# Performance work log

Measured on AMD Instinct MI355X. Metric: run time of the kernel, lower is better.

## Reference

```python
import jax, jax.numpy as jnp
import numpy as np

# xLSTM '80k' config: 4 blocks (mLSTM at 0,2,3; sLSTM at 1)
B, S, F = 128, 256, 10      # batch, seq (= context_length = forecast_horizon), features
E, NH = 40, 8               # d_model, heads
DH = E // NH                # 5,  sLSTM per-head dim
I = 128                     # mLSTM inner dim = round64(2*E)
QKB = 4; NQK = I // QKB     # q/k/v block-diagonal proj: 32 blocks of 4
MDH = I // NH               # 16, mLSTM per-head dim
FFD = 64                    # gated FFN dim = round64(1.3*E)
K = 4                       # causal conv kernel
NMB = 3                     # number of mLSTM blocks


def layer_norm(x, w, eps=1e-5):
    mu = x.mean(-1, keepdims=True)
    return (x - mu) * jax.lax.rsqrt(x.var(-1, keepdims=True) + eps) * w


def multihead_norm(x, w, nh, eps=1e-5):
    # per-head group norm over D//nh channels, weight only
    b, s, d = x.shape
    xh = x.reshape(b, s, nh, d // nh)
    xh = (xh - xh.mean(-1, keepdims=True)) * jax.lax.rsqrt(xh.var(-1, keepdims=True) + eps)
    return xh.reshape(b, s, d) * w


def causal_conv(x, w, b):
    # depthwise causal conv1d, kernel K; x: (B,S,C), w: (C,K)
    xt = x.transpose(0, 2, 1)
    y = jax.lax.conv_general_dilated(xt, w[:, None, :], (1,), [(K - 1, 0)],
                                     feature_group_count=x.shape[-1],
                                     dimension_numbers=('NCH', 'OIH', 'NCH'))
    return (y + b[None, :, None]).transpose(0, 2, 1)


def headwise(x, w):
    # block-diagonal linear (LinearHeadwiseExpand, no bias): w (nb, bo, bi)
    nb, bo, bi = w.shape
    xh = x.reshape(*x.shape[:-1], nb, bi)
    return jnp.einsum('bsni,noi->bsno', xh, w).reshape(*x.shape[:-1], nb * bo)


def pos_encoding():
    pos = jnp.arange(S, dtype=jnp.float32)[:, None]
    div = jnp.exp(jnp.arange(0, E, 2, dtype=jnp.float32) * (-np.log(10000.0) / E))
    pe = jnp.zeros((S, E), jnp.float32)
    pe = pe.at[:, 0::2].set(jnp.sin(pos * div))
    pe = pe.at[:, 1::2].set(jnp.cos(pos * div))
    return pe


def mlstm_layer(x, up_w, conv_w, conv_b, q_w, k_w, v_w, ig_w, ig_b, fg_w, fg_b, mhn_w, skip, down_w):
    x_m, z = jnp.split(x @ up_w.T, 2, axis=-1)                 # each (B,S,I)
    x_c = jax.nn.silu(causal_conv(x_m, conv_w, conv_b))
    q, k, v = headwise(x_c, q_w), headwise(x_c, k_w), headwise(x_m, v_w)
    gin = jnp.concatenate([q, k, v], axis=-1)                   # (B,S,3I)
    ip = (gin @ ig_w.T + ig_b).transpose(0, 2, 1)               # (B,NH,S)
    fp = (gin @ fg_w.T + fg_b).transpose(0, 2, 1)
    heads = lambda t: t.reshape(B, S, NH, MDH).transpose(0, 2, 1, 3)
    qh, kh, vh = heads(q), heads(k), heads(v)
    # stabilized parallel mLSTM (parallel_stabilized_simple)
    Fc = jnp.cumsum(jax.nn.log_sigmoid(fp), axis=-1)
    log_fg = Fc[..., :, None] - Fc[..., None, :]                # (B,NH,S,S)
    mask = jnp.tril(jnp.ones((S, S), bool))
    log_D = jnp.where(mask, log_fg, -jnp.inf) + ip[..., None, :]
    mD = jnp.max(log_D, axis=-1, keepdims=True)
    D = jnp.exp(log_D - mD)
    qk = jnp.einsum('bhsd,bhtd->bhst', qh, kh) * (MDH ** -0.5)
    C = qk * D
    nrm = jnp.maximum(jnp.abs(C.sum(-1, keepdims=True)), jnp.exp(-mD))
    h = jnp.einsum('bhst,bhtd->bhsd', C / (nrm + 1e-6), vh)
    h = multihead_norm(h.transpose(0, 2, 1, 3).reshape(B, S, I), mhn_w, NH)
    return ((h + skip * x_c) * jax.nn.silu(z)) @ down_w.T


def slstm_layer(x, conv_w, conv_b, wi, wf, wz, wo, R, bias, mhn_w):
    x_c = jax.nn.silu(causal_conv(x, conv_w, conv_b))
    g = lambda inp, w: headwise(inp, w).reshape(B, S, NH, DH)
    # i,f from conv path; z,o from raw input (order i,f,z,o)
    gx = jnp.stack([g(x_c, wi), g(x_c, wf), g(x, wz), g(x, wo)], axis=3)  # (B,S,NH,4,DH)
    gx = gx.transpose(1, 0, 2, 3, 4)                                      # (S,B,NH,4,DH)

    def step(carry, g_t):
        h, c, n, m = carry
        raw = g_t + jnp.einsum('bhd,hgde->bhge', h, R) + bias
        i_r, f_r, z_r, o_r = raw[:, :, 0], raw[:, :, 1], raw[:, :, 2], raw[:, :, 3]
        logfplusm = m + jax.nn.log_sigmoid(f_r)
        m_new = jnp.maximum(i_r, logfplusm)
        ig, fg = jnp.exp(i_r - m_new), jnp.exp(logfplusm - m_new)
        c_new = fg * c + ig * jnp.tanh(z_r)
        n_new = fg * n + ig
        h_new = jax.nn.sigmoid(o_r) * c_new / n_new
        return (h_new, c_new, n_new, m_new), h_new

    z0 = jnp.zeros((B, NH, DH), jnp.float32)
    _, hs = jax.lax.scan(step, (z0, z0, z0, z0), gx)
    return multihead_norm(hs.transpose(1, 0, 2, 3).reshape(B, S, E), mhn_w, NH)


def _forward(x, in_proj_w, in_proj_b, m_ln_w, m_up_w, m_conv_w, m_conv_b, m_q_w, m_k_w, m_v_w,
             m_ig_w, m_ig_b, m_fg_w, m_fg_b, m_mhn_w, m_skip, m_down_w,
             s_ln1_w, s_conv_w, s_conv_b, s_wi, s_wf, s_wz, s_wo, s_R, s_b, s_mhn_w,
             s_ln2_w, s_ff_up_w, s_ff_down_w, post_ln_w, out_w, out_b):
    h = x @ in_proj_w.T + in_proj_b + pos_encoding()
    mb = lambda h, j: h + mlstm_layer(layer_norm(h, m_ln_w[j]), m_up_w[j], m_conv_w[j], m_conv_b[j],
                                      m_q_w[j], m_k_w[j], m_v_w[j], m_ig_w[j], m_ig_b[j],
                                      m_fg_w[j], m_fg_b[j], m_mhn_w[j], m_skip[j], m_down_w[j])
    h = mb(h, 0)                       # block 0: mLSTM
    # block 1: sLSTM + gated FFN (pre-LN residual)
    h = h + slstm_layer(layer_norm(h, s_ln1_w), s_conv_w, s_conv_b, s_wi, s_wf, s_wz, s_wo, s_R, s_b, s_mhn_w)
    gpre, up = jnp.split(layer_norm(h, s_ln2_w) @ s_ff_up_w.T, 2, axis=-1)
    h = h + (jax.nn.gelu(gpre, approximate=False) * up) @ s_ff_down_w.T
    h = mb(h, 1)                       # block 2: mLSTM
    h = mb(h, 2)                       # block 3: mLSTM
    return layer_norm(h, post_ln_w) @ out_w.T + out_b


def setup_inputs():
    ks = iter(jax.random.split(jax.random.key(0), 64))
    rn = lambda shape, fan: jax.random.normal(next(ks), shape, jnp.float32) * (fan ** -0.5)
    d = {}
    d['x'] = jax.random.normal(next(ks), (B, S, F), jnp.float32)
    d['in_proj_w'] = rn((E, F), F); d['in_proj_b'] = jnp.zeros((E,), jnp.float32)
    d['m_ln_w'] = jnp.ones((NMB, E), jnp.float32)
    d['m_up_w'] = rn((NMB, 2 * I, E), E)
    d['m_conv_w'] = rn((NMB, I, K), K); d['m_conv_b'] = jnp.zeros((NMB, I), jnp.float32)
    d['m_q_w'] = rn((NMB, NQK, QKB, QKB), QKB)
    d['m_k_w'] = rn((NMB, NQK, QKB, QKB), QKB)
    d['m_v_w'] = rn((NMB, NQK, QKB, QKB), QKB)
    d['m_ig_w'] = rn((NMB, NH, 3 * I), 3 * I); d['m_ig_b'] = jnp.zeros((NMB, NH), jnp.float32)
    d['m_fg_w'] = rn((NMB, NH, 3 * I), 3 * I); d['m_fg_b'] = 3.0 * jnp.ones((NMB, NH), jnp.float32)
    d['m_mhn_w'] = jnp.ones((NMB, I), jnp.float32); d['m_skip'] = jnp.ones((NMB, I), jnp.float32)
    d['m_down_w'] = rn((NMB, E, I), I)
    d['s_ln1_w'] = jnp.ones((E,), jnp.float32)
    d['s_conv_w'] = rn((E, K), K); d['s_conv_b'] = jnp.zeros((E,), jnp.float32)
    d['s_wi'] = rn((NH, DH, DH), DH); d['s_wf'] = rn((NH, DH, DH), DH)
    d['s_wz'] = rn((NH, DH, DH), DH); d['s_wo'] = rn((NH, DH, DH), DH)
    d['s_R'] = rn((NH, 4, DH, DH), DH); d['s_b'] = jnp.zeros((NH, 4, DH), jnp.float32)
    d['s_mhn_w'] = jnp.ones((E,), jnp.float32); d['s_ln2_w'] = jnp.ones((E,), jnp.float32)
    d['s_ff_up_w'] = rn((2 * FFD, E), E); d['s_ff_down_w'] = rn((E, FFD), FFD)
    d['post_ln_w'] = jnp.ones((E,), jnp.float32)
    d['out_w'] = rn((1, E), E); d['out_b'] = jnp.zeros((1,), jnp.float32)
    return d


def reference(x, in_proj_w, in_proj_b, m_ln_w, m_up_w, m_conv_w, m_conv_b, m_q_w, m_k_w, m_v_w,
              m_ig_w, m_ig_b, m_fg_w, m_fg_b, m_mhn_w, m_skip, m_down_w,
              s_ln1_w, s_conv_w, s_conv_b, s_wi, s_wf, s_wz, s_wo, s_R, s_b, s_mhn_w,
              s_ln2_w, s_ff_up_w, s_ff_down_w, post_ln_w, out_w, out_b):
    return _forward(x, in_proj_w, in_proj_b, m_ln_w, m_up_w, m_conv_w, m_conv_b, m_q_w, m_k_w, m_v_w,
                    m_ig_w, m_ig_b, m_fg_w, m_fg_b, m_mhn_w, m_skip, m_down_w,
                    s_ln1_w, s_conv_w, s_conv_b, s_wi, s_wf, s_wz, s_wo, s_R, s_b, s_mhn_w,
                    s_ln2_w, s_ff_up_w, s_ff_down_w, post_ln_w, out_w, out_b)
```

## Files before the change

### kernel.cpp

```cpp
#include <hip/hip_runtime.h>
#include <math.h>

constexpr int cB = 128, cS = 256, cF = 10, cE = 40, cNH = 8, cDH = 5;
constexpr int cI = 128, cMDH = 16, cK = 4;

typedef __attribute__((ext_vector_type(8))) short short8v;
typedef __attribute__((ext_vector_type(4))) float f32x4;

#define BC8(v, l) __uint_as_float(__builtin_amdgcn_ds_swizzle(__float_as_uint(v), ((l) << 5) | 0x18))

__device__ __forceinline__ short f2bf(float f) {
    unsigned u = __float_as_uint(f);
    u += 0x7FFF + ((u >> 16) & 1);
    return (short)(u >> 16);
}

__global__ __launch_bounds__(256) void init_k(const float* __restrict__ x, const float* __restrict__ w,
                                              const float* __restrict__ b, float* __restrict__ h) {
    int idx = blockIdx.x * 256 + threadIdx.x;
    int e = idx % cE; int bs = idx / cE; int s = bs % cS;
    float acc = b[e];
    const float* xr = x + (size_t)bs * cF;
#pragma unroll
    for (int f = 0; f < cF; ++f) acc += xr[f] * w[e * cF + f];
    int i2 = e >> 1;
    float div = expf(-(float)(2 * i2) * (logf(10000.f) / 40.0f));
    float arg = (float)s * div;
    acc += (e & 1) ? cosf(arg) : sinf(arg);
    h[idx] = acc;
}

__global__ __launch_bounds__(256) void ln_up_k(const float* __restrict__ h, const float* __restrict__ lnw,
                                               const float* __restrict__ upw, float* __restrict__ xmz) {
    __shared__ float lnr[8][cE];
    int row0 = blockIdx.x * 8;
    int tid = threadIdx.x;
    if (tid < 8) {
        const float* r = h + (size_t)(row0 + tid) * cE;
        float mu = 0.f;
        for (int k = 0; k < cE; ++k) mu += r[k];
        mu *= (1.f / cE);
        float va = 0.f;
        for (int k = 0; k < cE; ++k) { float d = r[k] - mu; va += d * d; }
        va *= (1.f / cE);
        float rs = rsqrtf(va + 1e-5f);
        for (int k = 0; k < cE; ++k) lnr[tid][k] = (r[k] - mu) * rs * lnw[k];
    }
    __syncthreads();
    int o = tid;
    float acc[8] = {0, 0, 0, 0, 0, 0, 0, 0};
    for (int k = 0; k < cE; ++k) {
        float wv = upw[o * cE + k];
#pragma unroll
        for (int r = 0; r < 8; ++r) acc[r] += lnr[r][k] * wv;
    }
#pragma unroll
    for (int r = 0; r < 8; ++r) xmz[(size_t)(row0 + r) * 256 + o] = acc[r];
}

template <int C>
__global__ __launch_bounds__(256) void conv_silu_k(const float* __restrict__ in, int instride,
                                                   const float* __restrict__ w, const float* __restrict__ bias,
                                                   float* __restrict__ out) {
    int idx = blockIdx.x * 256 + threadIdx.x;
    int c = idx % C; int bs = idx / C; int s = bs % cS;
    float acc = bias[c];
#pragma unroll
    for (int j = 0; j < cK; ++j) {
        int sj = s - 3 + j;
        if (sj >= 0) acc += in[(size_t)(bs + j - 3) * instride + c] * w[c * cK + j];
    }
    float sg = 1.f / (1.f + __expf(-acc));
    out[idx] = acc * sg;
}

__global__ __launch_bounds__(256) void qkv_k(const float* __restrict__ xc, const float* __restrict__ xmz,
                                             const float* __restrict__ qw, const float* __restrict__ kw,
                                             const float* __restrict__ vw,
                                             float* __restrict__ qb, float* __restrict__ kb, float* __restrict__ vb) {
    int idx = blockIdx.x * 256 + threadIdx.x;
    int c = idx & 127; int bs = idx >> 7;
    int n = c >> 2, o = c & 3;
    const float* xcr = xc + (size_t)bs * cI + n * 4;
    const float* xmr = xmz + (size_t)bs * 256 + n * 4;
    const float* qwp = qw + n * 16 + o * 4;
    const float* kwp = kw + n * 16 + o * 4;
    const float* vwp = vw + n * 16 + o * 4;
    float aq = 0, ak = 0, av = 0;
#pragma unroll
    for (int i = 0; i < 4; ++i) { float a = xcr[i], m = xmr[i]; aq += a * qwp[i]; ak += a * kwp[i]; av += m * vwp[i]; }
    qb[idx] = aq; kb[idx] = ak; vb[idx] = av;
}

__global__ __launch_bounds__(128, 2) void gates_k(const float* __restrict__ qb, const float* __restrict__ kb,
                                                  const float* __restrict__ vb, const float* __restrict__ igw,
                                                  const float* __restrict__ igb, const float* __restrict__ fgw,
                                                  const float* __restrict__ fgb,
                                                  float* __restrict__ ipb, float* __restrict__ fpb) {
    __shared__ float g[32 * 388];
    __shared__ float w[16 * 388];
    int row0 = blockIdx.x * 32;
    int tid = threadIdx.x;

    for (int i = tid; i < 16 * 96; i += 128) {
        int r = i / 96, c4 = i - r * 96;
        const float* src = (r < 8) ? (igw + r * 384) : (fgw + (r - 8) * 384);
        *(float4*)&w[r * 388 + c4 * 4] = ((const float4*)src)[c4];
    }
    for (int i = tid; i < 32 * 96; i += 128) {
        int r = i / 96, c4 = i - r * 96;
        size_t gr = (size_t)(row0 + r) * cI;
        const float4* src = (c4 < 32) ? (const float4*)(qb + gr) + c4
                          : (c4 < 64) ? (const float4*)(kb + gr) + (c4 - 32)
                                      : (const float4*)(vb + gr) + (c4 - 64);
        *(float4*)&g[r * 388 + c4 * 4] = *src;
    }
    __syncthreads();

    int rp = tid >> 3;
    int hp = tid & 7;
    int r0 = 2 * rp, r1 = r0 + 1;
    int o0 = 2 * hp, o1 = o0 + 1;

    const float4* g0p = (const float4*)(g + r0 * 388);
    const float4* g1p = (const float4*)(g + r1 * 388);
    const float4* w0p = (const float4*)(w + o0 * 388);
    const float4* w1p = (const float4*)(w + o1 * 388);

    float a00 = 0.f, a01 = 0.f, a10 = 0.f, a11 = 0.f;
#pragma unroll 4
    for (int c4 = 0; c4 < 96; ++c4) {
        float4 gv0 = g0p[c4], gv1 = g1p[c4];
        float4 wv0 = w0p[c4], wv1 = w1p[c4];
        a00 = fmaf(gv0.x, wv0.x, a00); a00 = fmaf(gv0.y, wv0.y, a00);
        a00 = fmaf(gv0.z, wv0.z, a00); a00 = fmaf(gv0.w, wv0.w, a00);
        a01 = fmaf(gv0.x, wv1.x, a01); a01 = fmaf(gv0.y, wv1.y, a01);
        a01 = fmaf(gv0.z, wv1.z, a01); a01 = fmaf(gv0.w, wv1.w, a01);
        a10 = fmaf(gv1.x, wv0.x, a10); a10 = fmaf(gv1.y, wv0.y, a10);
        a10 = fmaf(gv1.z, wv0.z, a10); a10 = fmaf(gv1.w, wv0.w, a10);
        a11 = fmaf(gv1.x, wv1.x, a11); a11 = fmaf(gv1.y, wv1.y, a11);
        a11 = fmaf(gv1.z, wv1.z, a11); a11 = fmaf(gv1.w, wv1.w, a11);
    }

    int h0 = o0 & 7, wch0 = o0 >> 3;
    int h1 = o1 & 7, wch1 = o1 >> 3;
    float b0 = wch0 ? fgb[h0] : igb[h0];
    float b1 = wch1 ? fgb[h1] : igb[h1];
    int grow0 = row0 + r0, grow1 = row0 + r1;
    int bb0 = grow0 >> 8, ss0 = grow0 & 255;
    int bb1 = grow1 >> 8, ss1 = grow1 & 255;
    float* d00 = (wch0 ? fpb : ipb) + (size_t)(bb0 * cNH + h0) * cS + ss0;
    float* d01 = (wch1 ? fpb : ipb) + (size_t)(bb0 * cNH + h1) * cS + ss0;
    float* d10 = (wch0 ? fpb : ipb) + (size_t)(bb1 * cNH + h0) * cS + ss1;
    float* d11 = (wch1 ? fpb : ipb) + (size_t)(bb1 * cNH + h1) * cS + ss1;
    *d00 = a00 + b0; *d01 = a01 + b1; *d10 = a10 + b0; *d11 = a11 + b1;
}

constexpr int QKW = 24;
constexpr int VTW = 264;
constexpr int CBW = 280;

__global__ __launch_bounds__(256, 2) void attn_k(const float* __restrict__ qg, const float* __restrict__ kg,
                                                 const float* __restrict__ vg, const float* __restrict__ ipg,
                                                 const float* __restrict__ fpg, float* __restrict__ hatt) {
    int bh = blockIdx.x; int b = bh >> 3, h = bh & 7;
    int tid = threadIdx.x;
    int wid = tid >> 6, lane = tid & 63;
    int colL = lane & 15, grp = lane >> 4;

    __shared__ float sEA[cS], sMx[cS], sFc[cS];
    __shared__ short sQ[cS * QKW], sK[cS * QKW];
    __shared__ short sVt[cMDH * VTW];
    __shared__ short sC[4][16 * CBW];

    {
        const float4 fp4 = ((const float4*)(fpg + (size_t)bh * cS))[lane];
        const float4 ip4 = ((const float4*)(ipg + (size_t)bh * cS))[lane];
        float fpa[4] = {fp4.x, fp4.y, fp4.z, fp4.w};
        float ipa[4] = {ip4.x, ip4.y, ip4.z, ip4.w};
        float p[4];
        float run = 0.f;
#pragma unroll
        for (int i = 0; i < 4; ++i) {
            float xx = fpa[i];
            float lsg = fminf(xx, 0.f) - log1pf(expf(-fabsf(xx)));
            run += lsg; p[i] = run;
        }
        float cum = p[3];
#pragma unroll
        for (int off = 1; off < 64; off <<= 1) { float t = __shfl_up(cum, off); if (lane >= off) cum += t; }
        float excl = cum - p[3];
        float aa[4];
#pragma unroll
        for (int i = 0; i < 4; ++i) {
            float fcv = excl + p[i];
            aa[i] = ipa[i] - fcv;
            sFc[lane * 4 + i] = fcv;
            sEA[lane * 4 + i] = __expf(aa[i]);
        }
        float mq[4]; mq[0] = aa[0];
#pragma unroll
        for (int i = 1; i < 4; ++i) mq[i] = fmaxf(mq[i - 1], aa[i]);
        float cm = mq[3];
#pragma unroll
        for (int off = 1; off < 64; off <<= 1) { float t = __shfl_up(cm, off); if (lane >= off) cm = fmaxf(cm, t); }
        float exm = __shfl_up(cm, 1);
        if (lane == 0) exm = -3.0e38f;
#pragma unroll
        for (int i = 0; i < 4; ++i) sMx[lane * 4 + i] = fmaxf(exm, mq[i]);
    }

    {
        int t = tid;
        const float4* qp = (const float4*)(qg + ((size_t)(b * cS) + t) * cI + h * cMDH);
        const float4* kp = (const float4*)(kg + ((size_t)(b * cS) + t) * cI + h * cMDH);
        const float4* vp = (const float4*)(vg + ((size_t)(b * cS) + t) * cI + h * cMDH);
        float4 q0 = qp[0], q1 = qp[1], q2 = qp[2], q3 = qp[3];
        float4 k0 = kp[0], k1 = kp[1], k2 = kp[2], k3 = kp[3];
        float4 v0 = vp[0], v1 = vp[1], v2 = vp[2], v3 = vp[3];
        short8v qa, qbv, ka, kbv;
        qa[0] = f2bf(q0.x); qa[1] = f2bf(q0.y); qa[2] = f2bf(q0.z); qa[3] = f2bf(q0.w);
        qa[4] = f2bf(q1.x); qa[5] = f2bf(q1.y); qa[6] = f2bf(q1.z); qa[7] = f2bf(q1.w);
        qbv[0] = f2bf(q2.x); qbv[1] = f2bf(q2.y); qbv[2] = f2bf(q2.z); qbv[3] = f2bf(q2.w);
        qbv[4] = f2bf(q3.x); qbv[5] = f2bf(q3.y); qbv[6] = f2bf(q3.z); qbv[7] = f2bf(q3.w);
        ka[0] = f2bf(k0.x); ka[1] = f2bf(k0.y); ka[2] = f2bf(k0.z); ka[3] = f2bf(k0.w);
        ka[4] = f2bf(k1.x); ka[5] = f2bf(k1.y); ka[6] = f2bf(k1.z); ka[7] = f2bf(k1.w);
        kbv[0] = f2bf(k2.x); kbv[1] = f2bf(k2.y); kbv[2] = f2bf(k2.z); kbv[3] = f2bf(k2.w);
        kbv[4] = f2bf(k3.x); kbv[5] = f2bf(k3.y); kbv[6] = f2bf(k3.z); kbv[7] = f2bf(k3.w);
        *(short8v*)(sQ + t * QKW) = qa;
        *(short8v*)(sQ + t * QKW + 8) = qbv;
        *(short8v*)(sK + t * QKW) = ka;
        *(short8v*)(sK + t * QKW + 8) = kbv;
        sVt[0 * VTW + t] = f2bf(v0.x);  sVt[1 * VTW + t] = f2bf(v0.y);
        sVt[2 * VTW + t] = f2bf(v0.z);  sVt[3 * VTW + t] = f2bf(v0.w);
        sVt[4 * VTW + t] = f2bf(v1.x);  sVt[5 * VTW + t] = f2bf(v1.y);
        sVt[6 * VTW + t] = f2bf(v1.z);  sVt[7 * VTW + t] = f2bf(v1.w);
        sVt[8 * VTW + t] = f2bf(v2.x);  sVt[9 * VTW + t] = f2bf(v2.y);
        sVt[10 * VTW + t] = f2bf(v2.z); sVt[11 * VTW + t] = f2bf(v2.w);
        sVt[12 * VTW + t] = f2bf(v3.x); sVt[13 * VTW + t] = f2bf(v3.y);
        sVt[14 * VTW + t] = f2bf(v3.z); sVt[15 * VTW + t] = f2bf(v3.w);
    }
    __syncthreads();

    const short one_bf = (short)0x3F80;
    short8v ones = {one_bf, one_bf, one_bf, one_bf, one_bf, one_bf, one_bf, one_bf};
    short8v kz = {0, 0, 0, 0, 0, 0, 0, 0};
    short* Cb = sC[wid];

    for (int sti = 0; sti < 4; ++sti) {
        int st = wid + sti * 4;
        int s0 = st * 16;

        float eMx4[4], flr4[4];
#pragma unroll
        for (int j = 0; j < 4; ++j) {
            int sg = s0 + grp * 4 + j;
            eMx4[j] = 0.25f * __expf(-sMx[sg]);
            flr4[j] = __expf(-(sFc[sg] + sMx[sg]));
        }

        if ((st & 1) == 0) {
#pragma unroll
            for (int z = 0; z < 4; ++z) {
                int idx = lane * 4 + z;
                Cb[(idx >> 4) * CBW + (st + 1) * 16 + (idx & 15)] = 0;
            }
        }

        short8v aQ = (grp < 2) ? *(const short8v*)(sQ + (s0 + colL) * QKW + grp * 8) : kz;

        for (int tt = 0; tt <= st; ++tt) {
            int t0 = tt * 16;
            short8v bK = (grp < 2) ? *(const short8v*)(sK + (t0 + colL) * QKW + grp * 8) : kz;
            f32x4 zacc = {0.f, 0.f, 0.f, 0.f};
            f32x4 d = __builtin_amdgcn_mfma_f32_16x16x32_bf16(aQ, bK, zacc, 0, 0, 0);
            float ea = sEA[t0 + colL];
#pragma unroll
            for (int j = 0; j < 4; ++j) {
                float v = d[j] * (ea * eMx4[j]);
                if (tt == st) v = (colL <= grp * 4 + j) ? v : 0.f;
                Cb[(grp * 4 + j) * CBW + t0 + colL] = f2bf(v);
            }
        }

        __builtin_amdgcn_s_barrier();
        f32x4 hacc = {0.f, 0.f, 0.f, 0.f};
        f32x4 sacc = {0.f, 0.f, 0.f, 0.f};
        int nch = (st + 2) >> 1;
        for (int c = 0; c < nch; ++c) {
            int tc = c * 32;
            short8v aC = *(const short8v*)(Cb + colL * CBW + tc + grp * 8);
            short8v bV = *(const short8v*)(sVt + colL * VTW + tc + grp * 8);
            hacc = __builtin_amdgcn_mfma_f32_16x16x32_bf16(aC, bV, hacc, 0, 0, 0);
            sacc = __builtin_amdgcn_mfma_f32_16x16x32_bf16(aC, ones, sacc, 0, 0, 0);
        }

#pragma unroll
        for (int j = 0; j < 4; ++j) {
            int sg = s0 + grp * 4 + j;
            float nrm = fmaxf(fabsf(sacc[j]), flr4[j]) + 1e-6f;
            hatt[((size_t)(b * cS) + sg) * cI + h * cMDH + colL] = hacc[j] / nrm;
        }
    }
}

__global__ __launch_bounds__(320) void down_mhn_k(const float* __restrict__ hatt, const float* __restrict__ xc,
                                                  const float* __restrict__ xmz, const float* __restrict__ mhnw,
                                                  const float* __restrict__ skip, const float* __restrict__ dw,
                                                  float* __restrict__ h) {
    __shared__ float yl[8 * 128];
    int row0 = blockIdx.x * 8;
    int tid = threadIdx.x;
    for (int i = tid; i < 1024; i += 320) yl[i] = hatt[(size_t)row0 * cI + i];
    __syncthreads();
    if (tid < 64) {
        int r = tid >> 3, hh = tid & 7;
        int row = row0 + r;
        float* g = yl + r * 128 + hh * 16;
        float xv[16];
        float mu = 0.f;
#pragma unroll
        for (int d = 0; d < 16; ++d) { xv[d] = g[d]; mu += xv[d]; }
        mu *= (1.f / 16);
        float va = 0.f;
#pragma unroll
        for (int d = 0; d < 16; ++d) { float dd = xv[d] - mu; va += dd * dd; }
        va *= (1.f / 16);
        float rs = rsqrtf(va + 1e-5f);
        const float* xcr = xc + (size_t)row * cI + hh * 16;
        const float* zr  = xmz + (size_t)row * 256 + 128 + hh * 16;
#pragma unroll
        for (int d = 0; d < 16; ++d) {
            int i = hh * 16 + d;
            float z = zr[d];
            float sg = 1.f / (1.f + __expf(-z));
            g[d] = ((xv[d] - mu) * rs * mhnw[i] + skip[i] * xcr[d]) * (z * sg);
        }
    }
    __syncthreads();
    int r = tid / 40, e = tid % 40;
    const float* dr = dw + e * cI;
    const float* yr = yl + r * cI;
    float acc = 0.f;
    for (int i = 0; i < cI; ++i) acc += yr[i] * dr[i];
    h[(size_t)(row0 + r) * cE + e] += acc;
}

__global__ __launch_bounds__(256) void ln_rows_k(const float* __restrict__ h, const float* __restrict__ w,
                                                 float* __restrict__ out) {
    int rid = blockIdx.x * 256 + threadIdx.x;
    const float* r = h + (size_t)rid * cE;
    float mu = 0;
    for (int k = 0; k < cE; ++k) mu += r[k];
    mu *= (1.f / cE);
    float va = 0;
    for (int k = 0; k < cE; ++k) { float d = r[k] - mu; va += d * d; }
    va *= (1.f / cE);
    float rs = rsqrtf(va + 1e-5f);
    float* o = out + (size_t)rid * cE;
    for (int k = 0; k < cE; ++k) o[k] = (r[k] - mu) * rs * w[k];
}

__global__ __launch_bounds__(256) void sgates_k(const float* __restrict__ xcs, const float* __restrict__ ln1,
                                                const float* __restrict__ wi, const float* __restrict__ wf,
                                                const float* __restrict__ wz, const float* __restrict__ wo,
                                                float* __restrict__ gall) {
    int idx = blockIdx.x * 256 + threadIdx.x;
    int g = idx & 3; int r1 = idx >> 2;
    int e = r1 % 5; int r2 = r1 / 5;
    int bh = r2 & 1023; int s = r2 >> 10;
    int b = bh >> 3, h = bh & 7;
    const float* in = (g < 2) ? xcs : ln1;
    const float* w = (g == 0) ? wi : (g == 1) ? wf : (g == 2) ? wz : wo;
    const float* ir = in + ((size_t)(b * cS) + s) * cE + h * cDH;
    const float* wp = w + h * 25 + e * 5;
    float acc = 0.f;
#pragma unroll
    for (int i = 0; i < 5; ++i) acc += ir[i] * wp[i];
    gall[idx] = acc;
}

__global__ __launch_bounds__(64) void scan_k(const float* __restrict__ gall, const float* __restrict__ R,
                                             const float* __restrict__ bias, const float* __restrict__ mhnw,
                                             float* __restrict__ hbuf) {
    int lane = threadIdx.x;
    int grp = lane >> 3;
    int e = lane & 7;
    int ee = e < 5 ? e : 4;
    int bh = blockIdx.x * 8 + grp;
    int h = bh & 7;

    __shared__ float sOut[8][1285];

    float Rr[4][5];
#pragma unroll
    for (int g = 0; g < 4; ++g)
#pragma unroll
        for (int d = 0; d < 5; ++d) Rr[g][d] = R[h * 100 + g * 25 + d * 5 + ee];
    float bg[4];
#pragma unroll
    for (int g = 0; g < 4; ++g) bg[g] = bias[h * 20 + g * 5 + ee];
    float wmh = mhnw[h * 5 + ee];

    const float4* gp = (const float4*)gall + ((size_t)bh * 5 + ee);

    float4 rg[16];
#pragma unroll
    for (int j = 0; j < 16; ++j) rg[j] = gp[(size_t)j * 5120];

    float cstate = 0.f, nstate = 0.f, mstate = 0.f;
    float hs0 = 0.f, hs1 = 0.f, hs2 = 0.f, hs3 = 0.f, hs4 = 0.f;

    for (int t = 0; t < cS; t += 16) {
#pragma unroll
        for (int j = 0; j < 16; ++j) {
            float4 g4 = rg[j];
            rg[j] = gp[(size_t)(t + j + 16) * 5120];

            float ir = g4.x + bg[0], fr = g4.y + bg[1], zr = g4.z + bg[2], orr = g4.w + bg[3];
            ir = fmaf(hs0, Rr[0][0], ir); fr = fmaf(hs0, Rr[1][0], fr);
            zr = fmaf(hs0, Rr[2][0], zr); orr = fmaf(hs0, Rr[3][0], orr);
            ir = fmaf(hs1, Rr[0][1], ir); fr = fmaf(hs1, Rr[1][1], fr);
            zr = fmaf(hs1, Rr[2][1], zr); orr = fmaf(hs1, Rr[3][1], orr);
            ir = fmaf(hs2, Rr[0][2], ir); fr = fmaf(hs2, Rr[1][2], fr);
            zr = fmaf(hs2, Rr[2][2], zr); orr = fmaf(hs2, Rr[3][2], orr);
            ir = fmaf(hs3, Rr[0][3], ir); fr = fmaf(hs3, Rr[1][3], fr);
            zr = fmaf(hs3, Rr[2][3], zr); orr = fmaf(hs3, Rr[3][3], orr);
            ir = fmaf(hs4, Rr[0][4], ir); fr = fmaf(hs4, Rr[1][4], fr);
            zr = fmaf(hs4, Rr[2][4], zr); orr = fmaf(hs4, Rr[3][4], orr);

            float lsg = fminf(fr, 0.f) - __logf(1.f + __expf(-fabsf(fr)));
            float lfm = mstate + lsg;
            float mn = fmaxf(ir, lfm);
            float ig = __expf(ir - mn), fg = __expf(lfm - mn);
            float th = 1.f - 2.f * __builtin_amdgcn_rcpf(__expf(2.f * zr) + 1.f);
            float cn = fg * cstate + ig * th;
            float nn = fg * nstate + ig;
            float sg = __builtin_amdgcn_rcpf(1.f + __expf(-orr));
            float hn = sg * cn * __builtin_amdgcn_rcpf(nn);
            cstate = cn; nstate = nn; mstate = mn;

            hs0 = BC8(hn, 0); hs1 = BC8(hn, 1); hs2 = BC8(hn, 2);
            hs3 = BC8(hn, 3); hs4 = BC8(hn, 4);
            float mu = ((hs0 + hs1) + (hs2 + hs3) + hs4) * 0.2f;
            float d0 = hs0 - mu, d1 = hs1 - mu, d2 = hs2 - mu, d3 = hs3 - mu, d4 = hs4 - mu;
            float va = (d0 * d0 + d1 * d1 + d2 * d2 + d3 * d3 + d4 * d4) * 0.2f;
            float rs = __builtin_amdgcn_rsqf(va + 1e-5f);
            if (e < 5) sOut[grp][(t + j) * 5 + e] = (hn - mu) * rs * wmh;
        }
    }
    __syncthreads();

    for (int i = lane; i < 8 * 1280; i += 64) {
        int c = i / 1280;
        int r = i - c * 1280;
        int tt = r / 5, e2 = r - tt * 5;
        int bh2 = blockIdx.x * 8 + c;
        int b2 = bh2 >> 3, h2 = bh2 & 7;
        float* hp = hbuf + ((size_t)b2 * cS + tt) * cE + h2 * cDH + e2;
        *hp += sOut[c][r];
    }
}

__global__ __launch_bounds__(256) void ff1_k(const float* __restrict__ h, const float* __restrict__ lnw,
                                             const float* __restrict__ upw, float* __restrict__ ff) {
    __shared__ float lnr[4][cE];
    int row0 = blockIdx.x * 4;
    int tid = threadIdx.x;
    if (tid < 4) {
        const float* r = h + (size_t)(row0 + tid) * cE;
        float mu = 0;
        for (int k = 0; k < cE; ++k) mu += r[k];
        mu *= (1.f / cE);
        float va = 0;
        for (int k = 0; k < cE; ++k) { float d = r[k] - mu; va += d * d; }
        va *= (1.f / cE);
        float rs = rsqrtf(va + 1e-5f);
        for (int k = 0; k < cE; ++k) lnr[tid][k] = (r[k] - mu) * rs * lnw[k];
    }
    __syncthreads();
    int r = tid >> 6, f = tid & 63;
    float a = 0, u = 0;
    for (int k = 0; k < cE; ++k) {
        float xv = lnr[r][k];
        a += xv * upw[f * cE + k];
        u += xv * upw[(64 + f) * cE + k];
    }
    float g = 0.5f * a * (1.f + erff(a * 0.70710678118f));
    ff[(size_t)(row0 + r) * 64 + f] = g * u;
}

__global__ __launch_bounds__(320) void ff2_k(const float* __restrict__ ff, const float* __restrict__ dw,
                                             float* __restrict__ h) {
    __shared__ float fl[8 * 64];
    int row0 = blockIdx.x * 8;
    for (int i = threadIdx.x; i < 512; i += 320) fl[i] = ff[(size_t)row0 * 64 + i];
    __syncthreads();
    int r = threadIdx.x / 40, e = threadIdx.x % 40;
    const float* dr = dw + e * 64;
    const float* fr = fl + r * 64;
    float acc = 0.f;
    for (int i = 0; i < 64; ++i) acc += fr[i] * dr[i];
    h[(size_t)(row0 + r) * cE + e] += acc;
}

__global__ __launch_bounds__(256) void final_k(const float* __restrict__ h, const float* __restrict__ lnw,
                                               const float* __restrict__ ow, const float* __restrict__ ob,
                                               float* __restrict__ out) {
    int rid = blockIdx.x * 256 + threadIdx.x;
    const float* r = h + (size_t)rid * cE;
    float mu = 0;
    for (int k = 0; k < cE; ++k) mu += r[k];
    mu *= (1.f / cE);
    float va = 0;
    for (int k = 0; k < cE; ++k) { float d = r[k] - mu; va += d * d; }
    va *= (1.f / cE);
    float rs = rsqrtf(va + 1e-5f);
    float acc = ob[0];
    for (int k = 0; k < cE; ++k) acc += (r[k] - mu) * rs * lnw[k] * ow[k];
    out[rid] = acc;
}

extern "C" void kernel_launch(void* const* d_in, const int* in_sizes, int n_in,
                              void* d_out, int out_size, void* d_ws, size_t ws_size,
                              hipStream_t stream) {
    const float* x        = (const float*)d_in[0];
    const float* in_w     = (const float*)d_in[1];
    const float* in_b     = (const float*)d_in[2];
    const float* m_ln_w   = (const float*)d_in[3];
    const float* m_up_w   = (const float*)d_in[4];
    const float* m_conv_w = (const float*)d_in[5];
    const float* m_conv_b = (const float*)d_in[6];
    const float* m_q_w    = (const float*)d_in[7];
    const float* m_k_w    = (const float*)d_in[8];
    const float* m_v_w    = (const float*)d_in[9];
    const float* m_ig_w   = (const float*)d_in[10];
    const float* m_ig_b   = (const float*)d_in[11];
    const float* m_fg_w   = (const float*)d_in[12];
    const float* m_fg_b   = (const float*)d_in[13];
    const float* m_mhn_w  = (const float*)d_in[14];
    const float* m_skip   = (const float*)d_in[15];
    const float* m_down_w = (const float*)d_in[16];
    const float* s_ln1_w  = (const float*)d_in[17];
    const float* s_conv_w = (const float*)d_in[18];
    const float* s_conv_b = (const float*)d_in[19];
    const float* s_wi     = (const float*)d_in[20];
    const float* s_wf     = (const float*)d_in[21];
    const float* s_wz     = (const float*)d_in[22];
    const float* s_wo     = (const float*)d_in[23];
    const float* s_R      = (const float*)d_in[24];
    const float* s_bias   = (const float*)d_in[25];
    const float* s_mhn_w  = (const float*)d_in[26];
    const float* s_ln2_w  = (const float*)d_in[27];
    const float* s_ff_up  = (const float*)d_in[28];
    const float* s_ff_dn  = (const float*)d_in[29];
    const float* post_ln_w= (const float*)d_in[30];
    const float* out_w    = (const float*)d_in[31];
    const float* out_b    = (const float*)d_in[32];

    float* ws   = (float*)d_ws;
    float* h    = ws;
    float* xmz  = h + 1310720;
    float* xc   = xmz + 8388608;
    float* qb   = xc + 4194304;
    float* kb   = qb + 4194304;
    float* vb   = kb + 4194304;
    float* ipb  = vb + 4194304;
    float* fpb  = ipb + 262144;
    float* hatt = fpb + 262144;
    float* lnbuf = xmz;
    float* xcs   = xmz + 1310720;
    float* gall  = xmz + 2621440;
    float* ffbuf = xmz;

    init_k<<<5120, 256, 0, stream>>>(x, in_w, in_b, h);

    auto mlstm = [&](int j) {
        ln_up_k<<<4096, 256, 0, stream>>>(h, m_ln_w + j * cE, m_up_w + (size_t)j * 256 * cE, xmz);
        conv_silu_k<128><<<16384, 256, 0, stream>>>(xmz, 256, m_conv_w + j * cI * cK, m_conv_b + j * cI, xc);
        qkv_k<<<16384, 256, 0, stream>>>(xc, xmz, m_q_w + j * 512, m_k_w + j * 512, m_v_w + j * 512, qb, kb, vb);
        gates_k<<<1024, 128, 0, stream>>>(qb, kb, vb, m_ig_w + j * cNH * 384, m_ig_b + j * cNH,
                                          m_fg_w + j * cNH * 384, m_fg_b + j * cNH, ipb, fpb);
        attn_k<<<1024, 256, 0, stream>>>(qb, kb, vb, ipb, fpb, hatt);
        down_mhn_k<<<4096, 320, 0, stream>>>(hatt, xc, xmz, m_mhn_w + j * cI, m_skip + j * cI,
                                             m_down_w + j * cE * cI, h);
    };

    mlstm(0);

    ln_rows_k<<<128, 256, 0, stream>>>(h, s_ln1_w, lnbuf);
    conv_silu_k<40><<<5120, 256, 0, stream>>>(lnbuf, 40, s_conv_w, s_conv_b, xcs);
    sgates_k<<<20480, 256, 0, stream>>>(xcs, lnbuf, s_wi, s_wf, s_wz, s_wo, gall);
    scan_k<<<128, 64, 0, stream>>>(gall, s_R, s_bias, s_mhn_w, h);

    ff1_k<<<8192, 256, 0, stream>>>(h, s_ln2_w, s_ff_up, ffbuf);
    ff2_k<<<4096, 320, 0, stream>>>(ffbuf, s_ff_dn, h);

    mlstm(1);
    mlstm(2);

    final_k<<<128, 256, 0, stream>>>(h, post_ln_w, out_w, out_b, (float*)d_out);
}
```

Baseline: 892.7 us.

## Retile ln_up, widen gates block, balance attn tiles, drop per-tile barrier

ln_up_k now handles 16 rows per block and stages the up-projection weight transposed in shared memory, so the inner loop reads weights from LDS instead of strided global loads. gates_k runs 256 threads, one output row per thread pair, with two interleaved accumulators. attn_k gives each wave a balanced set of causal tiles (wid, 7-wid, 8+wid, 15-wid) instead of a strided set, and removes a workgroup barrier in the tile loop. The larger LDS footprint in ln_up_k may lower occupancy, and dropping the barrier relies on each wave using only its own Cb buffer.

```diff
diff --git a/kernel.cpp b/kernel.cpp
--- a/kernel.cpp
+++ b/kernel.cpp
@@ -32,10 +32,19 @@
 
 __global__ __launch_bounds__(256) void ln_up_k(const float* __restrict__ h, const float* __restrict__ lnw,
                                                const float* __restrict__ upw, float* __restrict__ xmz) {
-    __shared__ float lnr[8][cE];
-    int row0 = blockIdx.x * 8;
+    __shared__ float lnr[16][cE];
+    __shared__ float wT[cE * 257];
+    int row0 = blockIdx.x * 16;
     int tid = threadIdx.x;
-    if (tid < 8) {
+    for (int j = tid; j < 2560; j += 256) {
+        float4 v = ((const float4*)upw)[j];
+        int o = j / 10, kq = (j - o * 10) * 4;
+        wT[(kq + 0) * 257 + o] = v.x;
+        wT[(kq + 1) * 257 + o] = v.y;
+        wT[(kq + 2) * 257 + o] = v.z;
+        wT[(kq + 3) * 257 + o] = v.w;
+    }
+    if (tid < 16) {
         const float* r = h + (size_t)(row0 + tid) * cE;
         float mu = 0.f;
         for (int k = 0; k < cE; ++k) mu += r[k];
@@ -48,14 +57,16 @@
     }
     __syncthreads();
     int o = tid;
-    float acc[8] = {0, 0, 0, 0, 0, 0, 0, 0};
+    float acc[16];
+#pragma unroll
+    for (int r = 0; r < 16; ++r) acc[r] = 0.f;
     for (int k = 0; k < cE; ++k) {
-        float wv = upw[o * cE + k];
-#pragma unroll
-        for (int r = 0; r < 8; ++r) acc[r] += lnr[r][k] * wv;
-    }
-#pragma unroll
-    for (int r = 0; r < 8; ++r) xmz[(size_t)(row0 + r) * 256 + o] = acc[r];
+        float wv = wT[k * 257 + o];
+#pragma unroll
+        for (int r = 0; r < 16; ++r) acc[r] = fmaf(lnr[r][k], wv, acc[r]);
+    }
+#pragma unroll
+    for (int r = 0; r < 16; ++r) xmz[(size_t)(row0 + r) * 256 + o] = acc[r];
 }
 
 template <int C>
@@ -92,7 +103,7 @@
     qb[idx] = aq; kb[idx] = ak; vb[idx] = av;
 }
 
-__global__ __launch_bounds__(128, 2) void gates_k(const float* __restrict__ qb, const float* __restrict__ kb,
+__global__ __launch_bounds__(256, 2) void gates_k(const float* __restrict__ qb, const float* __restrict__ kb,
                                                   const float* __restrict__ vb, const float* __restrict__ igw,
                                                   const float* __restrict__ igb, const float* __restrict__ fgw,
                                                   const float* __restrict__ fgb,
@@ -102,12 +113,12 @@
     int row0 = blockIdx.x * 32;
     int tid = threadIdx.x;
 
-    for (int i = tid; i < 16 * 96; i += 128) {
+    for (int i = tid; i < 16 * 96; i += 256) {
         int r = i / 96, c4 = i - r * 96;
         const float* src = (r < 8) ? (igw + r * 384) : (fgw + (r - 8) * 384);
         *(float4*)&w[r * 388 + c4 * 4] = ((const float4*)src)[c4];
     }
-    for (int i = tid; i < 32 * 96; i += 128) {
+    for (int i = tid; i < 32 * 96; i += 256) {
         int r = i / 96, c4 = i - r * 96;
         size_t gr = (size_t)(row0 + r) * cI;
         const float4* src = (c4 < 32) ? (const float4*)(qb + gr) + c4
@@ -119,41 +130,38 @@
 
     int rp = tid >> 3;
     int hp = tid & 7;
-    int r0 = 2 * rp, r1 = r0 + 1;
     int o0 = 2 * hp, o1 = o0 + 1;
 
-    const float4* g0p = (const float4*)(g + r0 * 388);
-    const float4* g1p = (const float4*)(g + r1 * 388);
+    const float4* gp = (const float4*)(g + rp * 388);
     const float4* w0p = (const float4*)(w + o0 * 388);
     const float4* w1p = (const float4*)(w + o1 * 388);
 
-    float a00 = 0.f, a01 = 0.f, a10 = 0.f, a11 = 0.f;
-#pragma unroll 4
-    for (int c4 = 0; c4 < 96; ++c4) {
-        float4 gv0 = g0p[c4], gv1 = g1p[c4];
-        float4 wv0 = w0p[c4], wv1 = w1p[c4];
-        a00 = fmaf(gv0.x, wv0.x, a00); a00 = fmaf(gv0.y, wv0.y, a00);
-        a00 = fmaf(gv0.z, wv0.z, a00); a00 = fmaf(gv0.w, wv0.w, a00);
-        a01 = fmaf(gv0.x, wv1.x, a01); a01 = fmaf(gv0.y, wv1.y, a01);
-        a01 = fmaf(gv0.z, wv1.z, a01); a01 = fmaf(gv0.w, wv1.w, a01);
-        a10 = fmaf(gv1.x, wv0.x, a10); a10 = fmaf(gv1.y, wv0.y, a10);
-        a10 = fmaf(gv1.z, wv0.z, a10); a10 = fmaf(gv1.w, wv0.w, a10);
-        a11 = fmaf(gv1.x, wv1.x, a11); a11 = fmaf(gv1.y, wv1.y, a11);
-        a11 = fmaf(gv1.z, wv1.z, a11); a11 = fmaf(gv1.w, wv1.w, a11);
-    }
+    float a0e = 0.f, a0o = 0.f, a1e = 0.f, a1o = 0.f;
+#pragma unroll 2
+    for (int c4 = 0; c4 < 96; c4 += 2) {
+        float4 gv0 = gp[c4], gv1 = gp[c4 + 1];
+        float4 wa0 = w0p[c4], wa1 = w0p[c4 + 1];
+        float4 wb0 = w1p[c4], wb1 = w1p[c4 + 1];
+        a0e = fmaf(gv0.x, wa0.x, a0e); a0e = fmaf(gv0.y, wa0.y, a0e);
+        a0e = fmaf(gv0.z, wa0.z, a0e); a0e = fmaf(gv0.w, wa0.w, a0e);
+        a1e = fmaf(gv0.x, wb0.x, a1e); a1e = fmaf(gv0.y, wb0.y, a1e);
+        a1e = fmaf(gv0.z, wb0.z, a1e); a1e = fmaf(gv0.w, wb0.w, a1e);
+        a0o = fmaf(gv1.x, wa1.x, a0o); a0o = fmaf(gv1.y, wa1.y, a0o);
+        a0o = fmaf(gv1.z, wa1.z, a0o); a0o = fmaf(gv1.w, wa1.w, a0o);
+        a1o = fmaf(gv1.x, wb1.x, a1o); a1o = fmaf(gv1.y, wb1.y, a1o);
+        a1o = fmaf(gv1.z, wb1.z, a1o); a1o = fmaf(gv1.w, wb1.w, a1o);
+    }
+    float a0 = a0e + a0o, a1 = a1e + a1o;
 
     int h0 = o0 & 7, wch0 = o0 >> 3;
     int h1 = o1 & 7, wch1 = o1 >> 3;
     float b0 = wch0 ? fgb[h0] : igb[h0];
     float b1 = wch1 ? fgb[h1] : igb[h1];
-    int grow0 = row0 + r0, grow1 = row0 + r1;
-    int bb0 = grow0 >> 8, ss0 = grow0 & 255;
-    int bb1 = grow1 >> 8, ss1 = grow1 & 255;
-    float* d00 = (wch0 ? fpb : ipb) + (size_t)(bb0 * cNH + h0) * cS + ss0;
-    float* d01 = (wch1 ? fpb : ipb) + (size_t)(bb0 * cNH + h1) * cS + ss0;
-    float* d10 = (wch0 ? fpb : ipb) + (size_t)(bb1 * cNH + h0) * cS + ss1;
-    float* d11 = (wch1 ? fpb : ipb) + (size_t)(bb1 * cNH + h1) * cS + ss1;
-    *d00 = a00 + b0; *d01 = a01 + b1; *d10 = a10 + b0; *d11 = a11 + b1;
+    int grow = row0 + rp;
+    int bb = grow >> 8, ss = grow & 255;
+    float* d0 = (wch0 ? fpb : ipb) + (size_t)(bb * cNH + h0) * cS + ss;
+    float* d1 = (wch1 ? fpb : ipb) + (size_t)(bb * cNH + h1) * cS + ss;
+    *d0 = a0 + b0; *d1 = a1 + b1;
 }
 
 constexpr int QKW = 24;
@@ -246,9 +254,10 @@
     short8v ones = {one_bf, one_bf, one_bf, one_bf, one_bf, one_bf, one_bf, one_bf};
     short8v kz = {0, 0, 0, 0, 0, 0, 0, 0};
     short* Cb = sC[wid];
+    const int tiles[4] = {wid, 7 - wid, 8 + wid, 15 - wid};
 
     for (int sti = 0; sti < 4; ++sti) {
-        int st = wid + sti * 4;
+        int st = tiles[sti];
         int s0 = st * 16;
 
         float eMx4[4], flr4[4];
@@ -283,7 +292,6 @@
             }
         }
 
-        __builtin_amdgcn_s_barrier();
         f32x4 hacc = {0.f, 0.f, 0.f, 0.f};
         f32x4 sacc = {0.f, 0.f, 0.f, 0.f};
         int nch = (st + 2) >> 1;
@@ -576,10 +584,10 @@
     init_k<<<5120, 256, 0, stream>>>(x, in_w, in_b, h);
 
     auto mlstm = [&](int j) {
-        ln_up_k<<<4096, 256, 0, stream>>>(h, m_ln_w + j * cE, m_up_w + (size_t)j * 256 * cE, xmz);
+        ln_up_k<<<2048, 256, 0, stream>>>(h, m_ln_w + j * cE, m_up_w + (size_t)j * 256 * cE, xmz);
         conv_silu_k<128><<<16384, 256, 0, stream>>>(xmz, 256, m_conv_w + j * cI * cK, m_conv_b + j * cI, xc);
         qkv_k<<<16384, 256, 0, stream>>>(xc, xmz, m_q_w + j * 512, m_k_w + j * 512, m_v_w + j * 512, qb, kb, vb);
-        gates_k<<<1024, 128, 0, stream>>>(qb, kb, vb, m_ig_w + j * cNH * 384, m_ig_b + j * cNH,
+        gates_k<<<1024, 256, 0, stream>>>(qb, kb, vb, m_ig_w + j * cNH * 384, m_ig_b + j * cNH,
                                           m_fg_w + j * cNH * 384, m_fg_b + j * cNH, ipb, fpb);
         attn_k<<<1024, 256, 0, stream>>>(qb, kb, vb, ipb, fpb, hatt);
         down_mhn_k<<<4096, 320, 0, stream>>>(hatt, xc, xmz, m_mhn_w + j * cI, m_skip + j * cI,
```

After: 861.7 us. 1.04x faster.
